# Kernel tuning notes

Measured on AMD Instinct MI355X. Metric: run time of the kernel, lower is better.

## Reference

```python
import jax, jax.numpy as jnp
import numpy as np

HEADS = 16
HEAD_DIM = 64
EMB = 1024
B, S = 4, 2048
SCALE = 1.0 / 8.0  # fixed constant in the original code
MASK_PENALTY = -50.0  # original adds -50 * upper_triangular, not -inf


def setup_inputs() -> dict:
    key = jax.random.key(0)
    ks = jax.random.split(key, 5)
    x = jax.random.normal(ks[0], (B, S, EMB), dtype=jnp.float32)
    Wq = jax.random.normal(ks[1], (EMB, HEADS * HEAD_DIM), dtype=jnp.float32) * 0.02
    Wk = jax.random.normal(ks[2], (EMB, HEADS * HEAD_DIM), dtype=jnp.float32) * 0.02
    Wv = jax.random.normal(ks[3], (EMB, HEADS * HEAD_DIM), dtype=jnp.float32) * 0.02
    Wr = jax.random.normal(ks[4], (HEADS * HEAD_DIM, EMB), dtype=jnp.float32) * 0.02
    return {"x": x, "Wq": Wq, "Wk": Wk, "Wv": Wv, "Wr": Wr}


def reference(x, Wq, Wk, Wv, Wr):
    b, s, _ = x.shape
    # project and split heads: [b, s, h, d]
    q = (x @ Wq).reshape(b, s, HEADS, HEAD_DIM)
    k = (x @ Wk).reshape(b, s, HEADS, HEAD_DIM)
    v = (x @ Wv).reshape(b, s, HEADS, HEAD_DIM)
    # scores: [b, h, s, s]
    scores = SCALE * jnp.einsum('bqhd,bkhd->bhqk', q, k)
    # causal additive mask: -50 on strictly-upper triangle (faithful to original)
    causal = jnp.triu(jnp.ones((s, s), dtype=x.dtype), k=1)
    scores = scores + MASK_PENALTY * causal
    attn = jax.nn.softmax(scores, axis=-1)
    out = jnp.einsum('bhqk,bkhd->bqhd', attn, v).reshape(b, s, HEADS * HEAD_DIM)
    return out @ Wr
```

## Files before the change

kernel.cpp:

```cpp
#include <hip/hip_runtime.h>

typedef _Float16 f16;
typedef _Float16 f16x8 __attribute__((ext_vector_type(8)));
typedef _Float16 f16x4 __attribute__((ext_vector_type(4)));
typedef float f32x4 __attribute__((ext_vector_type(4)));
typedef float f32x16 __attribute__((ext_vector_type(16)));

#define MFMA16(A, B, C) __builtin_amdgcn_mfma_f32_16x16x32_f16((A), (B), (C), 0, 0, 0)
#define MFMA32(A, B, C) __builtin_amdgcn_mfma_f32_32x32x16_f16((A), (B), (C), 0, 0, 0)

__device__ __forceinline__ void async16(void* lds, const void* gp) {
    __builtin_amdgcn_global_load_lds(
        (__attribute__((address_space(1))) void*)(gp),
        (__attribute__((address_space(3))) void*)(lds), 16, 0, 0);
}

__global__ __launch_bounds__(256) void k_convert(const float* __restrict__ in,
                                                 f16* __restrict__ out, int n) {
    int i = (blockIdx.x * 256 + threadIdx.x) * 4;
    if (i + 3 < n) {
        float4 v = *(const float4*)(in + i);
        f16x4 o = {(f16)v.x, (f16)v.y, (f16)v.z, (f16)v.w};
        *(f16x4*)(out + i) = o;
    }
}

__global__ __launch_bounds__(256) void k_transpose_w4(const float* __restrict__ Wq,
                                                      const float* __restrict__ Wk,
                                                      const float* __restrict__ Wv,
                                                      const float* __restrict__ Wr,
                                                      f16* __restrict__ Wqkvt,
                                                      f16* __restrict__ Wrt) {
    __shared__ float tile[32][33];
    int z = blockIdx.z;
    const float* W = (z == 0) ? Wq : (z == 1) ? Wk : (z == 2) ? Wv : Wr;
    f16* Wt = (z == 3) ? Wrt : Wqkvt + z * 1048576;
    int c0 = blockIdx.x * 32, r0 = blockIdx.y * 32;
    int tx = threadIdx.x, ty = threadIdx.y;
#pragma unroll
    for (int j = 0; j < 32; j += 8)
        tile[ty + j][tx] = W[(r0 + ty + j) * 1024 + c0 + tx];
    __syncthreads();
#pragma unroll
    for (int j = 0; j < 32; j += 8)
        Wt[(c0 + ty + j) * 1024 + r0 + tx] = (f16)tile[tx][ty + j];
}

__global__ __launch_bounds__(256) void k_transpose_v(const f16* __restrict__ QKV,
                                                     f16* __restrict__ Vt) {
    __shared__ f16 tile[32][33];
    int s0 = blockIdx.x * 32;
    int d0 = blockIdx.y * 32;
    int bh = blockIdx.z;
    int b = bh >> 4, h = bh & 15;
    int tx = threadIdx.x, ty = threadIdx.y;
#pragma unroll
    for (int j = 0; j < 32; j += 8)
        tile[ty + j][tx] = QKV[(b * 2048 + s0 + ty + j) * 3072 + 2048 + h * 64 + d0 + tx];
    __syncthreads();
#pragma unroll
    for (int j = 0; j < 32; j += 8)
        Vt[(bh * 64 + d0 + ty + j) * 2048 + s0 + tx] = tile[tx][ty + j];
}

template <bool OUT_F16>
__global__ __launch_bounds__(256, 4) void k_gemm_bt(const f16* __restrict__ A,
                                                    const f16* __restrict__ Bt,
                                                    void* __restrict__ Cv,
                                                    int M, int N, int K) {
    __shared__ f16 As[128][32];
    __shared__ f16 Bs[128][32];
    int t = threadIdx.x;
    int lane = t & 63, w = t >> 6;
    int wm = (w >> 1) * 64, wn = (w & 1) * 64;
    int m0 = blockIdx.y * 128, n0 = blockIdx.x * 128;
    int ln = lane & 31, kh = lane >> 5;
    int sw = (ln >> 1) & 3;

    int lin0 = w * 128 + lane, lin1 = lin0 + 64;
    int r0 = lin0 >> 2, c0 = (lin0 & 3) ^ ((r0 >> 1) & 3);
    int r1 = lin1 >> 2, c1 = (lin1 & 3) ^ ((r1 >> 1) & 3);
    const f16* gA0 = A + (size_t)(m0 + r0) * K + c0 * 8;
    const f16* gA1 = A + (size_t)(m0 + r1) * K + c1 * 8;
    const f16* gB0 = Bt + (size_t)(n0 + r0) * K + c0 * 8;
    const f16* gB1 = Bt + (size_t)(n0 + r1) * K + c1 * 8;
    f16* lA0 = &As[0][0] + w * 1024;
    f16* lB0 = &Bs[0][0] + w * 1024;

    f32x16 acc[2][2] = {};

    for (int k0 = 0; k0 < K; k0 += 32) {
        __syncthreads();
        async16(lA0, gA0 + k0);
        async16(lA0 + 512, gA1 + k0);
        async16(lB0, gB0 + k0);
        async16(lB0 + 512, gB1 + k0);
        __syncthreads();
#pragma unroll
        for (int kd = 0; kd < 2; kd++) {
            int c = kd * 2 + kh;
            f16x8 af[2], bf[2];
#pragma unroll
            for (int mt = 0; mt < 2; mt++)
                af[mt] = *(const f16x8*)&As[wm + mt * 32 + ln][(c ^ sw) * 8];
#pragma unroll
            for (int nt = 0; nt < 2; nt++)
                bf[nt] = *(const f16x8*)&Bs[wn + nt * 32 + ln][(c ^ sw) * 8];
#pragma unroll
            for (int mt = 0; mt < 2; mt++)
#pragma unroll
                for (int nt = 0; nt < 2; nt++)
                    acc[mt][nt] = MFMA32(af[mt], bf[nt], acc[mt][nt]);
        }
    }

#pragma unroll
    for (int mt = 0; mt < 2; mt++)
#pragma unroll
        for (int nt = 0; nt < 2; nt++)
#pragma unroll
            for (int r = 0; r < 16; r++) {
                int row = m0 + wm + mt * 32 + (r & 3) + 8 * (r >> 2) + 4 * kh;
                int col = n0 + wn + nt * 32 + ln;
                float v = acc[mt][nt][r];
                if (OUT_F16)
                    ((f16*)Cv)[(size_t)row * N + col] = (f16)v;
                else
                    ((float*)Cv)[(size_t)row * N + col] = v;
            }
}

__global__ __launch_bounds__(256, 4) void k_attn(const f16* __restrict__ QKV,
                                                 const f16* __restrict__ Vt,
                                                 f16* __restrict__ Ob) {
    __shared__ f16 Ks[64][72];
    __shared__ f16 Vs[64][72];
    __shared__ f16 Ps[128][72];
    int bh = blockIdx.x;
    int qt = 15 - (int)blockIdx.y;
    int b = bh >> 4, h = bh & 15;
    int q0 = qt * 128;
    int t = threadIdx.x, lane = t & 63, wq = t >> 6;
    int ln = lane & 15, g = lane >> 4, g8 = g * 8, rg = g * 4;

    int c0 = t, c1 = t + 256;
    int kr0 = c0 >> 3, kc0 = (c0 & 7) * 8;
    int kr1 = c1 >> 3, kc1 = (c1 & 7) * 8;
    const f16* Kbase = QKV + (size_t)b * 2048 * 3072 + 1024 + h * 64;
    const f16* Vbase = Vt + (size_t)bh * 64 * 2048;

    const float C_SCL = 0.18033688f;
    const float C_MSK = -72.134752f;
    f16x8 ones;
#pragma unroll
    for (int j = 0; j < 8; j++) ones[j] = (f16)1.f;

    f16x8 bq[2][2];
#pragma unroll
    for (int nt = 0; nt < 2; nt++)
#pragma unroll
        for (int kd = 0; kd < 2; kd++)
            bq[nt][kd] = *(const f16x8*)(QKV +
                (size_t)(b * 2048 + q0 + wq * 32 + nt * 16 + ln) * 3072 +
                h * 64 + kd * 32 + g8);

    int4 rk0 = *(const int4*)(Kbase + (size_t)kr0 * 3072 + kc0);
    int4 rk1 = *(const int4*)(Kbase + (size_t)kr1 * 3072 + kc1);
    int4 rv0 = *(const int4*)(Vbase + (size_t)kr0 * 2048 + kc0);
    int4 rv1 = *(const int4*)(Vbase + (size_t)kr1 * 2048 + kc1);

    f32x4 oacc[2][4] = {};
    f32x4 osum[2] = {};
    int nk = q0 / 64 + 2;

    for (int kt = 0; kt < nk; kt++) {
        int k0 = kt * 64;
        __syncthreads();
        *(int4*)&Ks[kr0][kc0] = rk0;
        *(int4*)&Ks[kr1][kc1] = rk1;
        *(int4*)&Vs[kr0][kc0] = rv0;
        *(int4*)&Vs[kr1][kc1] = rv1;
        if (kt + 1 < nk) {
            int kn = k0 + 64;
            rk0 = *(const int4*)(Kbase + (size_t)(kn + kr0) * 3072 + kc0);
            rk1 = *(const int4*)(Kbase + (size_t)(kn + kr1) * 3072 + kc1);
            rv0 = *(const int4*)(Vbase + (size_t)kr0 * 2048 + kn + kc0);
            rv1 = *(const int4*)(Vbase + (size_t)kr1 * 2048 + kn + kc1);
        }
        __syncthreads();

        if (k0 > q0 + wq * 32 + 31) continue;

        f32x4 sacc[4][2] = {};
#pragma unroll
        for (int kd = 0; kd < 2; kd++) {
            f16x8 ak[4];
#pragma unroll
            for (int mt = 0; mt < 4; mt++)
                ak[mt] = *(const f16x8*)&Ks[mt * 16 + ln][kd * 32 + g8];
#pragma unroll
            for (int mt = 0; mt < 4; mt++)
#pragma unroll
                for (int nt = 0; nt < 2; nt++)
                    sacc[mt][nt] = MFMA16(ak[mt], bq[nt][kd], sacc[mt][nt]);
        }

        bool needs_mask = (k0 + 63 > q0 + wq * 32);
#pragma unroll
        for (int nt = 0; nt < 2; nt++) {
            int q = q0 + wq * 32 + nt * 16 + ln;
#pragma unroll
            for (int mt = 0; mt < 4; mt++) {
                f16x4 pk;
#pragma unroll
                for (int r = 0; r < 4; r++) {
                    float e;
                    if (needs_mask) {
                        int kk = k0 + mt * 16 + rg + r;
                        e = __builtin_amdgcn_exp2f(
                            fmaf(sacc[mt][nt][r], C_SCL, (kk > q) ? C_MSK : 0.f));
                    } else {
                        e = __builtin_amdgcn_exp2f(sacc[mt][nt][r] * C_SCL);
                    }
                    pk[r] = (f16)e;
                }
                *(f16x4*)&Ps[wq * 32 + nt * 16 + ln][mt * 16 + rg] = pk;
            }
        }

#pragma unroll
        for (int kk = 0; kk < 2; kk++) {
            f16x8 ap[2], bv[4];
#pragma unroll
            for (int mt = 0; mt < 2; mt++)
                ap[mt] = *(const f16x8*)&Ps[wq * 32 + mt * 16 + ln][kk * 32 + g8];
#pragma unroll
            for (int dt = 0; dt < 4; dt++)
                bv[dt] = *(const f16x8*)&Vs[dt * 16 + ln][kk * 32 + g8];
#pragma unroll
            for (int mt = 0; mt < 2; mt++) {
#pragma unroll
                for (int dt = 0; dt < 4; dt++)
                    oacc[mt][dt] = MFMA16(ap[mt], bv[dt], oacc[mt][dt]);
                osum[mt] = MFMA16(ap[mt], ones, osum[mt]);
            }
        }
    }

#pragma unroll
    for (int mt = 0; mt < 2; mt++)
#pragma unroll
        for (int r = 0; r < 4; r++) {
            float inv = __builtin_amdgcn_rcpf(osum[mt][r]);
            int row = b * 2048 + q0 + wq * 32 + mt * 16 + rg + r;
#pragma unroll
            for (int dt = 0; dt < 4; dt++)
                Ob[(size_t)row * 1024 + h * 64 + dt * 16 + ln] =
                    (f16)(oacc[mt][dt][r] * inv);
        }
}

extern "C" void kernel_launch(void* const* d_in, const int* in_sizes, int n_in,
                              void* d_out, int out_size, void* d_ws, size_t ws_size,
                              hipStream_t stream) {
    const float* x = (const float*)d_in[0];
    const float* Wq = (const float*)d_in[1];
    const float* Wk = (const float*)d_in[2];
    const float* Wv = (const float*)d_in[3];
    const float* Wr = (const float*)d_in[4];
    float* out = (float*)d_out;

    f16* ws = (f16*)d_ws;
    f16* xb    = ws;
    f16* Wqkvt = xb + 8388608;
    f16* Wrt   = Wqkvt + 3145728;
    f16* QKVb  = Wrt + 1048576;
    f16* Vtb   = QKVb + 25165824;
    f16* Obuf  = Vtb + 8388608;

    k_convert<<<8192, 256, 0, stream>>>(x, xb, 8388608);
    dim3 tb(32, 8);
    k_transpose_w4<<<dim3(32, 32, 4), tb, 0, stream>>>(Wq, Wk, Wv, Wr, Wqkvt, Wrt);
    k_gemm_bt<true><<<dim3(24, 64), 256, 0, stream>>>(xb, Wqkvt, QKVb, 8192, 3072, 1024);
    k_transpose_v<<<dim3(64, 2, 64), tb, 0, stream>>>(QKVb, Vtb);
    k_attn<<<dim3(64, 16), 256, 0, stream>>>(QKVb, Vtb, Obuf);
    k_gemm_bt<false><<<dim3(8, 64), 256, 0, stream>>>(Obuf, Wrt, out, 8192, 1024, 1024);
}
```

Baseline: 294.5 us.

## Keep P in registers via 16x16x16 MFMA and double attention query tile

The attention kernel now feeds the softmax probabilities straight from registers into a 16x16x16 MFMA, whose accumulator layout matches its A-operand layout, so the P staging buffer in shared memory and its write/read round trip are removed. Each wave now covers 64 queries instead of 32, and each block 256 instead of 128, which halves the number of times K/V tiles are loaded per query. Query tiles are scheduled in an interleaved heavy/light order to balance the causal work. The cost is more registers per thread (occupancy hint lowered from 4 to 2), half as many blocks, and K=16 MFMAs with lower throughput per instruction.

```diff
diff --git a/kernel.cpp b/kernel.cpp
--- a/kernel.cpp
+++ b/kernel.cpp
@@ -8,6 +8,7 @@
 
 #define MFMA16(A, B, C) __builtin_amdgcn_mfma_f32_16x16x32_f16((A), (B), (C), 0, 0, 0)
 #define MFMA32(A, B, C) __builtin_amdgcn_mfma_f32_32x32x16_f16((A), (B), (C), 0, 0, 0)
+#define MFMA16K16(A, B, C) __builtin_amdgcn_mfma_f32_16x16x16f16((A), (B), (C), 0, 0, 0)
 
 __device__ __forceinline__ void async16(void* lds, const void* gp) {
     __builtin_amdgcn_global_load_lds(
@@ -130,48 +131,45 @@
             }
 }
 
-__global__ __launch_bounds__(256, 4) void k_attn(const f16* __restrict__ QKV,
+__global__ __launch_bounds__(256, 2) void k_attn(const f16* __restrict__ QKV,
                                                  const f16* __restrict__ Vt,
                                                  f16* __restrict__ Ob) {
     __shared__ f16 Ks[64][72];
     __shared__ f16 Vs[64][72];
-    __shared__ f16 Ps[128][72];
     int bh = blockIdx.x;
-    int qt = 15 - (int)blockIdx.y;
+    int y = blockIdx.y;
+    int qt = (y < 4) ? (7 - y) : (y - 4);
     int b = bh >> 4, h = bh & 15;
-    int q0 = qt * 128;
+    int q0 = qt * 256;
     int t = threadIdx.x, lane = t & 63, wq = t >> 6;
     int ln = lane & 15, g = lane >> 4, g8 = g * 8, rg = g * 4;
-
-    int c0 = t, c1 = t + 256;
-    int kr0 = c0 >> 3, kc0 = (c0 & 7) * 8;
-    int kr1 = c1 >> 3, kc1 = (c1 & 7) * 8;
+    int qw = q0 + wq * 64;
+
+    int kr0 = t >> 3, kc0 = (t & 7) * 8;
+    int kr1 = (t + 256) >> 3, kc1 = (t & 7) * 8;
     const f16* Kbase = QKV + (size_t)b * 2048 * 3072 + 1024 + h * 64;
     const f16* Vbase = Vt + (size_t)bh * 64 * 2048;
 
     const float C_SCL = 0.18033688f;
     const float C_MSK = -72.134752f;
-    f16x8 ones;
-#pragma unroll
-    for (int j = 0; j < 8; j++) ones[j] = (f16)1.f;
-
-    f16x8 bq[2][2];
-#pragma unroll
-    for (int nt = 0; nt < 2; nt++)
+    f16x4 ones4 = {(f16)1.f, (f16)1.f, (f16)1.f, (f16)1.f};
+
+    f16x8 bq[4][2];
+#pragma unroll
+    for (int nt = 0; nt < 4; nt++)
 #pragma unroll
         for (int kd = 0; kd < 2; kd++)
             bq[nt][kd] = *(const f16x8*)(QKV +
-                (size_t)(b * 2048 + q0 + wq * 32 + nt * 16 + ln) * 3072 +
-                h * 64 + kd * 32 + g8);
+                (size_t)(b * 2048 + qw + nt * 16 + ln) * 3072 + h * 64 + kd * 32 + g8);
 
     int4 rk0 = *(const int4*)(Kbase + (size_t)kr0 * 3072 + kc0);
     int4 rk1 = *(const int4*)(Kbase + (size_t)kr1 * 3072 + kc1);
     int4 rv0 = *(const int4*)(Vbase + (size_t)kr0 * 2048 + kc0);
     int4 rv1 = *(const int4*)(Vbase + (size_t)kr1 * 2048 + kc1);
 
-    f32x4 oacc[2][4] = {};
-    f32x4 osum[2] = {};
-    int nk = q0 / 64 + 2;
+    f32x4 oacc[4][4] = {};
+    f32x4 osum[4] = {};
+    int nk = 4 * qt + 4;
 
     for (int kt = 0; kt < nk; kt++) {
         int k0 = kt * 64;
@@ -189,9 +187,9 @@
         }
         __syncthreads();
 
-        if (k0 > q0 + wq * 32 + 31) continue;
-
-        f32x4 sacc[4][2] = {};
+        if (k0 > qw + 63) continue;
+
+        f32x4 sacc[4][4] = {};
 #pragma unroll
         for (int kd = 0; kd < 2; kd++) {
             f16x8 ak[4];
@@ -201,17 +199,17 @@
 #pragma unroll
             for (int mt = 0; mt < 4; mt++)
 #pragma unroll
-                for (int nt = 0; nt < 2; nt++)
+                for (int nt = 0; nt < 4; nt++)
                     sacc[mt][nt] = MFMA16(ak[mt], bq[nt][kd], sacc[mt][nt]);
         }
 
-        bool needs_mask = (k0 + 63 > q0 + wq * 32);
-#pragma unroll
-        for (int nt = 0; nt < 2; nt++) {
-            int q = q0 + wq * 32 + nt * 16 + ln;
+        bool needs_mask = (k0 + 63 > qw);
+        f16x4 pk[4][4];
+#pragma unroll
+        for (int nt = 0; nt < 4; nt++) {
+            int q = qw + nt * 16 + ln;
 #pragma unroll
             for (int mt = 0; mt < 4; mt++) {
-                f16x4 pk;
 #pragma unroll
                 for (int r = 0; r < 4; r++) {
                     float e;
@@ -222,41 +220,37 @@
                     } else {
                         e = __builtin_amdgcn_exp2f(sacc[mt][nt][r] * C_SCL);
                     }
-                    pk[r] = (f16)e;
+                    pk[mt][nt][r] = (f16)e;
                 }
-                *(f16x4*)&Ps[wq * 32 + nt * 16 + ln][mt * 16 + rg] = pk;
             }
         }
 
 #pragma unroll
-        for (int kk = 0; kk < 2; kk++) {
-            f16x8 ap[2], bv[4];
-#pragma unroll
-            for (int mt = 0; mt < 2; mt++)
-                ap[mt] = *(const f16x8*)&Ps[wq * 32 + mt * 16 + ln][kk * 32 + g8];
+        for (int mt = 0; mt < 4; mt++) {
+            f16x4 bv[4];
 #pragma unroll
             for (int dt = 0; dt < 4; dt++)
-                bv[dt] = *(const f16x8*)&Vs[dt * 16 + ln][kk * 32 + g8];
-#pragma unroll
-            for (int mt = 0; mt < 2; mt++) {
+                bv[dt] = *(const f16x4*)&Vs[dt * 16 + ln][mt * 16 + rg];
+#pragma unroll
+            for (int nt = 0; nt < 4; nt++) {
 #pragma unroll
                 for (int dt = 0; dt < 4; dt++)
-                    oacc[mt][dt] = MFMA16(ap[mt], bv[dt], oacc[mt][dt]);
-                osum[mt] = MFMA16(ap[mt], ones, osum[mt]);
+                    oacc[nt][dt] = MFMA16K16(pk[mt][nt], bv[dt], oacc[nt][dt]);
+                osum[nt] = MFMA16K16(pk[mt][nt], ones4, osum[nt]);
             }
         }
     }
 
 #pragma unroll
-    for (int mt = 0; mt < 2; mt++)
+    for (int nt = 0; nt < 4; nt++)
 #pragma unroll
         for (int r = 0; r < 4; r++) {
-            float inv = __builtin_amdgcn_rcpf(osum[mt][r]);
-            int row = b * 2048 + q0 + wq * 32 + mt * 16 + rg + r;
+            float inv = __builtin_amdgcn_rcpf(osum[nt][r]);
+            int row = b * 2048 + qw + nt * 16 + rg + r;
 #pragma unroll
             for (int dt = 0; dt < 4; dt++)
                 Ob[(size_t)row * 1024 + h * 64 + dt * 16 + ln] =
-                    (f16)(oacc[mt][dt][r] * inv);
+                    (f16)(oacc[nt][dt][r] * inv);
         }
 }
 
@@ -283,6 +277,6 @@
     k_transpose_w4<<<dim3(32, 32, 4), tb, 0, stream>>>(Wq, Wk, Wv, Wr, Wqkvt, Wrt);
     k_gemm_bt<true><<<dim3(24, 64), 256, 0, stream>>>(xb, Wqkvt, QKVb, 8192, 3072, 1024);
     k_transpose_v<<<dim3(64, 2, 64), tb, 0, stream>>>(QKVb, Vtb);
-    k_attn<<<dim3(64, 16), 256, 0, stream>>>(QKVb, Vtb, Obuf);
+    k_attn<<<dim3(64, 8), 256, 0, stream>>>(QKVb, Vtb, Obuf);
     k_gemm_bt<false><<<dim3(8, 64), 256, 0, stream>>>(Obuf, Wrt, out, 8192, 1024, 1024);
 }
```

After: 290.6 us. About the same (-1.3%).
